# Optimization experiments

Hardware: AMD Instinct MI355X
Metric: run time of the kernel (lower is better)

## Reference

```python
import jax, jax.numpy as jnp
import numpy as np

N = 100000   # nodes
E = 800000   # edges
IN = 128     # in_channels == embedding_size (required by residual Linear)
EMB = 128
OUT = 64
EPS = 1e-5   # GraphNorm eps (PyG default)


def setup_inputs() -> dict:
    key = jax.random.key(0)
    ks = jax.random.split(key, 8)
    x = jax.random.normal(ks[0], (N, IN), jnp.float32)
    edge_index = jax.random.randint(ks[1], (2, E), 0, N, dtype=jnp.int64)
    g = lambda k, shape, scale: jax.random.normal(k, shape, jnp.float32) * scale
    return dict(
        x=x,
        edge_index=edge_index,
        W1=g(ks[2], (IN, EMB), IN ** -0.5), b1=jnp.zeros((EMB,), jnp.float32),
        W2=g(ks[3], (EMB, EMB), EMB ** -0.5), b2=jnp.zeros((EMB,), jnp.float32),
        gn1_w=1.0 + g(ks[4], (EMB,), 0.05), gn1_b=jnp.zeros((EMB,), jnp.float32), gn1_ms=jnp.ones((EMB,), jnp.float32),
        gn2_w=1.0 + g(ks[5], (EMB,), 0.05), gn2_b=jnp.zeros((EMB,), jnp.float32), gn2_ms=jnp.ones((EMB,), jnp.float32),
        Wr=g(ks[6], (EMB, OUT), EMB ** -0.5), br=jnp.zeros((OUT,), jnp.float32),
    )


def _gcn_conv(x, W, b, src, dst, dinv):
    # PyG GCNConv: h = x @ W; out[i] = sum_{(j->i)} dinv[j]*dinv[i]*h[j]; out += bias
    h = x @ W
    norm = (dinv[src] * dinv[dst])[:, None]        # [E+N, 1]
    msg = h[src] * norm                             # gather + scale (irregular)
    out = jax.ops.segment_sum(msg, dst, num_segments=N)  # scatter-add
    return out + b


def _graph_norm(h, w, b, ms):
    # PyG GraphNorm, single graph: mean/var over node dim
    mean = jnp.mean(h, axis=0)
    c = h - ms * mean
    var = jnp.mean(c * c, axis=0)
    return w * c * jax.lax.rsqrt(var + EPS) + b


def reference(x, edge_index, W1, b1, W2, b2, gn1_w, gn1_b, gn1_ms, gn2_w, gn2_b, gn2_ms, Wr, br):
    loops = jnp.arange(N, dtype=edge_index.dtype)
    src = jnp.concatenate([edge_index[0], loops])   # add self-loops
    dst = jnp.concatenate([edge_index[1], loops])
    deg = jax.ops.segment_sum(jnp.ones_like(src, dtype=x.dtype), dst, num_segments=N)
    dinv = jnp.where(deg > 0, jax.lax.rsqrt(jnp.maximum(deg, 1.0)), 0.0)

    # dropout is identity in eval mode
    x1 = jax.nn.relu(_graph_norm(_gcn_conv(x, W1, b1, src, dst, dinv), gn1_w, gn1_b, gn1_ms))
    x2 = jax.nn.relu(_graph_norm(_gcn_conv(x1, W2, b2, src, dst, dinv), gn2_w, gn2_b, gn2_ms))
    return (x1 + x2) @ Wr + br
```

## Files before the change

### kernel.cpp

```cpp
#include <hip/hip_runtime.h>
#include <hip/hip_bf16.h>

typedef __attribute__((ext_vector_type(8))) short bf16x8;
typedef __attribute__((ext_vector_type(4))) float f32x4;
typedef __attribute__((ext_vector_type(2))) float f32x2;
typedef __attribute__((ext_vector_type(4))) unsigned int u32x4;

#define STATS_BLOCKS 256
#define SLOTS 32

__device__ __forceinline__ int coh_load(const int* p){
  return __hip_atomic_load(p, __ATOMIC_RELAXED, __HIP_MEMORY_SCOPE_AGENT);
}
__device__ __forceinline__ unsigned int coh_loadu(const unsigned int* p){
  return __hip_atomic_load(p, __ATOMIC_RELAXED, __HIP_MEMORY_SCOPE_AGENT);
}

__device__ __forceinline__ float bf2f(unsigned short u){
  union { unsigned int i; float f; } v; v.i = ((unsigned int)u) << 16; return v.f;
}
__device__ __forceinline__ unsigned short f2bf(float f){
  union { float f; unsigned int i; } v; v.f = f;
  return (unsigned short)((v.i + 0x7fffu + ((v.i >> 16) & 1u)) >> 16);
}
__device__ __forceinline__ f32x2 bf2x(unsigned int w){
  union { unsigned int i; float f; } lo, hi;
  lo.i = w << 16; hi.i = w & 0xffff0000u;
  f32x2 r; r.x = lo.f; r.y = hi.f; return r;
}


__global__ __launch_bounds__(256) void k_setup(
    const float* __restrict__ W1, const float* __restrict__ W2, const float* __restrict__ Wr,
    unsigned short* __restrict__ wp1, unsigned short* __restrict__ wp2,
    unsigned short* __restrict__ wpr,
    const int* __restrict__ dst, int* __restrict__ hist, int E, int NBUK){
  int b = blockIdx.x;
  if (b < 160){
    int pb = b;
    const float* W; unsigned short* wp; int ncols;
    if (pb < 64)      { W = W1; wp = wp1; ncols = 128; }
    else if (pb < 128){ W = W2; wp = wp2; ncols = 128; pb -= 64; }
    else              { W = Wr; wp = wpr; ncols = 64;  pb -= 128; }
    int idx = pb*256 + threadIdx.x;
    if (idx >= 128*ncols) return;
    int bb = idx & 7, lane = (idx>>3)&63, kk = (idx>>9)&3, ct = idx>>11;
    int k = kk*32 + ((lane>>4)<<3) + bb;
    int c = ct*16 + (lane&15);
    wp[idx] = f2bf(W[k*ncols + c]);
    return;
  }
  int c = b - 160;
  __shared__ int hcnt[256];
  hcnt[threadIdx.x] = 0;
  __syncthreads();
  int per = (E + 255) >> 8;
  int e0 = c*per, e1 = min(E, e0 + per);
  for (int e = e0 + threadIdx.x; e < e1; e += 256)
    atomicAdd(&hcnt[dst[e] >> 9], 1);
  __syncthreads();
  int t = threadIdx.x;
  if (t < NBUK) hist[t*256 + c] = hcnt[t];
}


__global__ __launch_bounds__(256) void k_scanA(int* __restrict__ hist,
                                               int* __restrict__ btot){
  int b = blockIdx.x, t = threadIdx.x;
  int v = hist[b*256 + t];
  __shared__ int sh[256];
  sh[t] = v; __syncthreads();
  for (int o = 1; o < 256; o <<= 1){
    int x = (t >= o) ? sh[t-o] : 0;
    __syncthreads();
    sh[t] += x;
    __syncthreads();
  }
  hist[b*256 + t] = sh[t] - v;
  if (t == 255) btot[b] = sh[255];
}


__global__ __launch_bounds__(256) void k_scatter(const int* __restrict__ src,
    const int* __restrict__ dst, const int* __restrict__ hist,
    const int* __restrict__ btot, unsigned int* __restrict__ ebuf, int E, int NBUK){
  __shared__ int sh[256];
  __shared__ int cursor[256];
  int c = blockIdx.x, t = threadIdx.x;
  int v = (t < NBUK) ? btot[t] : 0;
  sh[t] = v; __syncthreads();
  for (int o = 1; o < 256; o <<= 1){
    int x = (t >= o) ? sh[t-o] : 0;
    __syncthreads();
    sh[t] += x;
    __syncthreads();
  }
  if (t < NBUK) cursor[t] = hist[t*256 + c] + (sh[t] - v);
  __syncthreads();
  int per = (E + 255) >> 8;
  int e0 = c*per, e1 = min(E, e0 + per);
  for (int e = e0 + t; e < e1; e += 256){
    int d = dst[e], s = src[e];
    int bin = d >> 9;
    int pos = atomicAdd(&cursor[bin], 1);
    ebuf[pos] = ((unsigned int)(d & 511) << 17) | (unsigned int)s;
  }
}


__global__ __launch_bounds__(256) void k_bucket(const unsigned int* __restrict__ ebuf,
    const int* __restrict__ btot, int* __restrict__ cur, int* __restrict__ col,
    int N, int NBUK){
  __shared__ int sh[256];
  __shared__ int cnt[512];
  int b = blockIdx.x, t = threadIdx.x;
  int v = (t < NBUK) ? btot[t] : 0;
  sh[t] = v;
  cnt[t] = 0; cnt[t + 256] = 0;
  __syncthreads();
  for (int o = 1; o < 256; o <<= 1){
    int x = (t >= o) ? sh[t-o] : 0;
    __syncthreads();
    sh[t] += x;
    __syncthreads();
  }
  int e1 = sh[b];
  int e0 = e1 - btot[b];
  int base = b << 9;
  for (int e = e0 + t; e < e1; e += 256){
    unsigned int w = coh_loadu(&ebuf[e]);
    int dl = (int)(w >> 17);
    int s  = (int)(w & 0x1FFFFu);
    int p = atomicAdd(&cnt[dl], 1);
    if (p < SLOTS) col[(size_t)(base + dl)*SLOTS + p] = s;
  }
  __syncthreads();
  int d0 = base + t, d1 = base + t + 256;
  if (d0 < N) cur[d0] = cnt[t];
  if (d1 < N) cur[d1] = cnt[t + 256];
}


__global__ __launch_bounds__(256) void k_gemm1(const float* __restrict__ A,
    const unsigned short* __restrict__ wp, const int* __restrict__ cur,
    unsigned short* __restrict__ h, int nTiles){
  int gw = (int)((blockIdx.x*256 + threadIdx.x) >> 6);
  if (gw >= nTiles) return;
  int lane = threadIdx.x & 63;
  int row0 = gw*16;
  int r  = row0 + (lane & 15);
  int kb = (lane >> 4) * 8;
  bf16x8 a[4];
#pragma unroll
  for (int kk = 0; kk < 4; ++kk){
    const float* p = A + (size_t)r*128 + kk*32 + kb;
    f32x4 v0 = *reinterpret_cast<const f32x4*>(p);
    f32x4 v1 = *reinterpret_cast<const f32x4*>(p + 4);
#pragma unroll
    for (int b = 0; b < 4; ++b){ a[kk][b] = (short)f2bf(v0[b]); a[kk][4+b] = (short)f2bf(v1[b]); }
  }
  int cst = lane & 15;
  int rb  = row0 + ((lane >> 4) << 2);
  float dv[4];
#pragma unroll
  for (int b2 = 0; b2 < 4; ++b2) dv[b2] = rsqrtf(1.0f + (float)cur[rb + b2]);
#pragma unroll
  for (int ct = 0; ct < 8; ++ct){
    f32x4 acc = {0.f,0.f,0.f,0.f};
#pragma unroll
    for (int kk = 0; kk < 4; ++kk){
      bf16x8 b = *reinterpret_cast<const bf16x8*>(wp + ((ct*4 + kk)*64 + lane)*8);
      acc = __builtin_amdgcn_mfma_f32_16x16x32_bf16(a[kk], b, acc, 0, 0, 0);
    }
    int c = ct*16 + cst;
#pragma unroll
    for (int b2 = 0; b2 < 4; ++b2)
      h[(size_t)(rb + b2)*128 + c] = f2bf(dv[b2]*acc[b2]);
  }
}


__global__ __launch_bounds__(256) void k_agg(const unsigned short* __restrict__ h,
    const int* __restrict__ cur, const int* col,
    const float* __restrict__ bias, unsigned short* __restrict__ agg, int N){
  int gw = (int)((blockIdx.x*256 + threadIdx.x) >> 6);
  if (gw*2 >= N) return;
  int lane = threadIdx.x & 63;
  int i = gw*2 + (lane >> 5);
  if (i >= N) i = N - 1;
  int q  = (lane >> 4) & 1;
  int cl = lane & 15;
  int base = lane & 32;
  const u32x4* hp = reinterpret_cast<const u32x4*>(h);
  int craw = cur[i];
  int colv = coh_load(&col[(size_t)i*SLOTS + (lane & 31)]);
  int c = min(craw, SLOTS);
  int idx = ((lane & 31) < c) ? colv : i;
  f32x2 a0 = {0.f,0.f}, a1 = {0.f,0.f}, a2 = {0.f,0.f}, a3 = {0.f,0.f};
  int j = 0;
  for (; j + 4 <= c; j += 4){
    int r0 = __shfl(idx, base + j + q);
    int r1 = __shfl(idx, base + j + 2 + q);
    u32x4 v0 = hp[(size_t)r0*16 + cl];
    u32x4 v1 = hp[(size_t)r1*16 + cl];
    a0 += bf2x(v0.x) + bf2x(v1.x);
    a1 += bf2x(v0.y) + bf2x(v1.y);
    a2 += bf2x(v0.z) + bf2x(v1.z);
    a3 += bf2x(v0.w) + bf2x(v1.w);
  }
  int rem = c - j;
  if (rem > 0){
    int r0 = __shfl(idx, base + j + q);
    int r1 = __shfl(idx, base + j + 2 + q);
    if (q < rem){
      u32x4 v0 = hp[(size_t)r0*16 + cl];
      a0 += bf2x(v0.x); a1 += bf2x(v0.y); a2 += bf2x(v0.z); a3 += bf2x(v0.w);
    }
    if (q + 2 < rem){
      u32x4 v1 = hp[(size_t)r1*16 + cl];
      a0 += bf2x(v1.x); a1 += bf2x(v1.y); a2 += bf2x(v1.z); a3 += bf2x(v1.w);
    }
  }
  float acc[8] = {a0.x, a0.y, a1.x, a1.y, a2.x, a2.y, a3.x, a3.y};
#pragma unroll
  for (int b = 0; b < 8; ++b)
    acc[b] += __shfl_xor(acc[b], 16);
  if ((lane & 16) == 0){
    u32x4 hv = hp[(size_t)i*16 + cl];
    float di = rsqrtf(1.0f + (float)craw);
    f32x4 bb0 = *reinterpret_cast<const f32x4*>(bias + cl*8);
    f32x4 bb1 = *reinterpret_cast<const f32x4*>(bias + cl*8 + 4);
    f32x2 s0 = bf2x(hv.x), s1 = bf2x(hv.y), s2 = bf2x(hv.z), s3 = bf2x(hv.w);
    float sf[8] = {s0.x, s0.y, s1.x, s1.y, s2.x, s2.y, s3.x, s3.y};
    float fin[8];
#pragma unroll
    for (int b = 0; b < 4; ++b) fin[b] = di*(acc[b] + sf[b]) + bb0[b];
#pragma unroll
    for (int b = 0; b < 4; ++b) fin[4+b] = di*(acc[4+b] + sf[4+b]) + bb1[b];
    u32x4 ov;
    asm("v_cvt_pk_bf16_f32 %0, %1, %2" : "=v"(ov.x) : "v"(fin[0]), "v"(fin[1]));
    asm("v_cvt_pk_bf16_f32 %0, %1, %2" : "=v"(ov.y) : "v"(fin[2]), "v"(fin[3]));
    asm("v_cvt_pk_bf16_f32 %0, %1, %2" : "=v"(ov.z) : "v"(fin[4]), "v"(fin[5]));
    asm("v_cvt_pk_bf16_f32 %0, %1, %2" : "=v"(ov.w) : "v"(fin[6]), "v"(fin[7]));
    reinterpret_cast<u32x4*>(agg)[(size_t)i*16 + cl] = ov;
  }
}


__global__ __launch_bounds__(256) void k_stats(const unsigned short* __restrict__ agg,
    float* __restrict__ partials, int N){
  int tid = blockIdx.x*256 + threadIdx.x;
  int g = threadIdx.x & 15;
  int c0 = g * 8;
  float S1[8] = {0,0,0,0,0,0,0,0}, S2[8] = {0,0,0,0,0,0,0,0};
  size_t total = (size_t)N * 16;
  for (size_t p = tid; p < total; p += (size_t)STATS_BLOCKS*256){
    bf16x8 v = reinterpret_cast<const bf16x8*>(agg)[p];
#pragma unroll
    for (int b = 0; b < 8; ++b){
      float f = bf2f((unsigned short)v[b]);
      S1[b] += f; S2[b] += f*f;
    }
  }
  __shared__ float sh1[16][128];
  __shared__ float sh2[16][128];
  int cp = threadIdx.x >> 4;
#pragma unroll
  for (int b = 0; b < 8; ++b){ sh1[cp][c0 + b] = S1[b]; sh2[cp][c0 + b] = S2[b]; }
  __syncthreads();
  int t = threadIdx.x;
  if (t < 128){
    float s = 0.f;
#pragma unroll
    for (int qq = 0; qq < 16; ++qq) s += sh1[qq][t];
    partials[blockIdx.x*256 + t] = s;
  } else {
    int cc = t - 128;
    float s = 0.f;
#pragma unroll
    for (int qq = 0; qq < 16; ++qq) s += sh2[qq][cc];
    partials[blockIdx.x*256 + 128 + cc] = s;
  }
}


__global__ void k_reduce(const float* __restrict__ partials, const float* __restrict__ gw_,
    const float* __restrict__ gb_, const float* __restrict__ gms_,
    float* __restrict__ st, int N){
  int t = threadIdx.x;
  float S = 0.f;
#pragma unroll 8
  for (int b = 0; b < STATS_BLOCKS; ++b)
    S += partials[b*256 + t];
  __shared__ float sh[256];
  sh[t] = S;
  __syncthreads();
  if (t >= 128) return;
  int c = t;
  float S1 = sh[c], S2 = sh[128 + c];
  float m  = S1 / (float)N;
  float ms = gms_[c];
  float var = S2/(float)N - 2.f*ms*m*m + ms*ms*m*m;
  float rs = rsqrtf(var + 1e-5f);
  float wv = gw_[c];
  st[c]       = wv * rs;
  st[128 + c] = gb_[c] - wv*rs*ms*m;
}


__global__ __launch_bounds__(256) void k_gemm2(const unsigned short* __restrict__ agg,
    const float* __restrict__ st, const unsigned short* __restrict__ wp,
    const int* __restrict__ cur, unsigned short* __restrict__ h, int nTiles){
  int gw = (int)((blockIdx.x*256 + threadIdx.x) >> 6);
  if (gw >= nTiles) return;
  int lane = threadIdx.x & 63;
  int row0 = gw*16;
  int r  = row0 + (lane & 15);
  int kb = (lane >> 4) * 8;
  bf16x8 a[4];
#pragma unroll
  for (int kk = 0; kk < 4; ++kk){
    int cb = kk*32 + kb;
    bf16x8 v = *reinterpret_cast<const bf16x8*>(agg + (size_t)r*128 + cb);
    f32x4 s0 = *reinterpret_cast<const f32x4*>(st + cb);
    f32x4 s1 = *reinterpret_cast<const f32x4*>(st + cb + 4);
    f32x4 t0 = *reinterpret_cast<const f32x4*>(st + 128 + cb);
    f32x4 t1 = *reinterpret_cast<const f32x4*>(st + 128 + cb + 4);
#pragma unroll
    for (int b = 0; b < 4; ++b){
      a[kk][b]   = (short)f2bf(fmaxf(0.f, s0[b]*bf2f((unsigned short)v[b])   + t0[b]));
      a[kk][4+b] = (short)f2bf(fmaxf(0.f, s1[b]*bf2f((unsigned short)v[4+b]) + t1[b]));
    }
  }
  int cst = lane & 15;
  int rb  = row0 + ((lane >> 4) << 2);
  float dv[4];
#pragma unroll
  for (int b2 = 0; b2 < 4; ++b2) dv[b2] = rsqrtf(1.0f + (float)cur[rb + b2]);
#pragma unroll
  for (int ct = 0; ct < 8; ++ct){
    f32x4 acc = {0.f,0.f,0.f,0.f};
#pragma unroll
    for (int kk = 0; kk < 4; ++kk){
      bf16x8 b = *reinterpret_cast<const bf16x8*>(wp + ((ct*4 + kk)*64 + lane)*8);
      acc = __builtin_amdgcn_mfma_f32_16x16x32_bf16(a[kk], b, acc, 0, 0, 0);
    }
    int c = ct*16 + cst;
#pragma unroll
    for (int b2 = 0; b2 < 4; ++b2)
      h[(size_t)(rb + b2)*128 + c] = f2bf(dv[b2]*acc[b2]);
  }
}


__global__ __launch_bounds__(256) void k_final(const unsigned short* __restrict__ agg1,
    const unsigned short* __restrict__ agg2, const float* __restrict__ st,
    const unsigned short* __restrict__ wp, const float* __restrict__ br,
    float* __restrict__ out, int nTiles){
  int gw = (int)((blockIdx.x*256 + threadIdx.x) >> 6);
  if (gw >= nTiles) return;
  int lane = threadIdx.x & 63;
  int row0 = gw*16;
  int r  = row0 + (lane & 15);
  int kb = (lane >> 4) * 8;
  bf16x8 a[4];
#pragma unroll
  for (int kk = 0; kk < 4; ++kk){
    int cb = kk*32 + kb;
    bf16x8 g1 = *reinterpret_cast<const bf16x8*>(agg1 + (size_t)r*128 + cb);
    bf16x8 g2 = *reinterpret_cast<const bf16x8*>(agg2 + (size_t)r*128 + cb);
#pragma unroll
    for (int b = 0; b < 8; ++b){
      int c = cb + b;
      float x1v = bf2f(f2bf(fmaxf(0.f, st[c]*bf2f((unsigned short)g1[b]) + st[128 + c])));
      float r2  = fmaxf(0.f, st[256 + c]*bf2f((unsigned short)g2[b]) + st[384 + c]);
      a[kk][b] = (short)f2bf(x1v + r2);
    }
  }
  int cst = lane & 15;
  int rb  = row0 + ((lane >> 4) << 2);
#pragma unroll
  for (int ct = 0; ct < 4; ++ct){
    f32x4 acc = {0.f,0.f,0.f,0.f};
#pragma unroll
    for (int kk = 0; kk < 4; ++kk){
      bf16x8 b = *reinterpret_cast<const bf16x8*>(wp + ((ct*4 + kk)*64 + lane)*8);
      acc = __builtin_amdgcn_mfma_f32_16x16x32_bf16(a[kk], b, acc, 0, 0, 0);
    }
    int c = ct*16 + cst;
    float bias = br[c];
#pragma unroll
    for (int b2 = 0; b2 < 4; ++b2)
      out[(size_t)(rb + b2)*64 + c] = acc[b2] + bias;
  }
}


extern "C" void kernel_launch(void* const* d_in, const int* in_sizes, int n_in,
                              void* d_out, int out_size, void* d_ws, size_t ws_size,
                              hipStream_t stream){
  const float* x    = (const float*)d_in[0];
  const int*   ei   = (const int*)d_in[1];
  const float* W1   = (const float*)d_in[2];
  const float* b1   = (const float*)d_in[3];
  const float* W2   = (const float*)d_in[4];
  const float* b2   = (const float*)d_in[5];
  const float* g1w  = (const float*)d_in[6];
  const float* g1b  = (const float*)d_in[7];
  const float* g1ms = (const float*)d_in[8];
  const float* g2w  = (const float*)d_in[9];
  const float* g2b  = (const float*)d_in[10];
  const float* g2ms = (const float*)d_in[11];
  const float* Wr   = (const float*)d_in[12];
  const float* br   = (const float*)d_in[13];
  float* out = (float*)d_out;

  int N = in_sizes[0] / 128;
  int E = in_sizes[1] / 2;
  const int* srcp = ei;
  const int* dstp = ei + E;

  char* w = (char*)d_ws;
  auto alloc = [&](size_t bytes){ char* p = w; w += (bytes + 255) & ~(size_t)255; return p; };
  int*   cur           = (int*)  alloc((size_t)N*4);
  int*   col           = (int*)  alloc((size_t)N*SLOTS*4);
  int*   hist          = (int*)  alloc(256*256*4);
  int*   btot          = (int*)  alloc(256*4);
  unsigned int* ebuf   = (unsigned int*)alloc((size_t)E*4);
  float* partials      = (float*)alloc((size_t)STATS_BLOCKS*256*4);
  float* st            = (float*)alloc(4*128*4);
  unsigned short* wp1  = (unsigned short*)alloc(128*128*2);
  unsigned short* wp2  = (unsigned short*)alloc(128*128*2);
  unsigned short* wpr  = (unsigned short*)alloc(128*64*2);
  unsigned short* h    = (unsigned short*)alloc((size_t)N*128*2);
  unsigned short* agg1 = (unsigned short*)alloc((size_t)N*128*2);
  unsigned short* agg2 = (unsigned short*)alloc((size_t)N*128*2);

  int nTiles = N / 16;
  int gemmBlocks = (nTiles + 3) / 4;
  int NBUK = (N + 511) >> 9;
  int aggBlocks = (N + 7) / 8;

  k_setup  <<<160 + 256, 256, 0, stream>>>(W1, W2, Wr, wp1, wp2, wpr, dstp, hist, E, NBUK);
  k_scanA  <<<NBUK, 256, 0, stream>>>(hist, btot);
  k_scatter<<<256, 256, 0, stream>>>(srcp, dstp, hist, btot, ebuf, E, NBUK);
  k_bucket <<<NBUK, 256, 0, stream>>>(ebuf, btot, cur, col, N, NBUK);

  k_gemm1<<<gemmBlocks, 256, 0, stream>>>(x, wp1, cur, h, nTiles);
  k_agg  <<<aggBlocks, 256, 0, stream>>>(h, cur, col, b1, agg1, N);
  k_stats<<<STATS_BLOCKS, 256, 0, stream>>>(agg1, partials, N);
  k_reduce<<<1, 256, 0, stream>>>(partials, g1w, g1b, g1ms, st, N);

  k_gemm2<<<gemmBlocks, 256, 0, stream>>>(agg1, st, wp2, cur, h, nTiles);
  k_agg  <<<aggBlocks, 256, 0, stream>>>(h, cur, col, b2, agg2, N);
  k_stats<<<STATS_BLOCKS, 256, 0, stream>>>(agg2, partials, N);
  k_reduce<<<1, 256, 0, stream>>>(partials, g2w, g2b, g2ms, st + 256, N);

  k_final<<<gemmBlocks, 256, 0, stream>>>(agg1, agg2, st, wpr, br, out, nTiles);
}
```

Baseline: 206.2 us.

## Fuse GraphNorm statistics into aggregation and remap aggregation to four nodes per wave

The aggregation kernel now handles four nodes per wave, with 16 lanes per node, instead of two nodes split across half-waves. This removes the cross-half shuffle reduction and the partial-tail logic. The per-channel sum and sum-of-squares for GraphNorm are computed in-block from the fp32 results and written as per-block partials, which removes the separate stats pass that re-read the aggregated output. A two-stage reduction (64 blocks, then 1) replaces the single-block reduce. The trade-off is less memory-level parallelism per node, a shared-memory reduction plus syncthreads in every agg block, and a large partials buffer. Stats also now come from pre-rounding fp32 values rather than the stored bf16.

```diff
diff --git a/kernel.cpp b/kernel.cpp
--- a/kernel.cpp
+++ b/kernel.cpp
@@ -6,7 +6,6 @@
 typedef __attribute__((ext_vector_type(2))) float f32x2;
 typedef __attribute__((ext_vector_type(4))) unsigned int u32x4;
 
-#define STATS_BLOCKS 256
 #define SLOTS 32
 
 __device__ __forceinline__ int coh_load(const int* p){
@@ -182,25 +181,29 @@
 
 __global__ __launch_bounds__(256) void k_agg(const unsigned short* __restrict__ h,
     const int* __restrict__ cur, const int* col,
-    const float* __restrict__ bias, unsigned short* __restrict__ agg, int N){
-  int gw = (int)((blockIdx.x*256 + threadIdx.x) >> 6);
-  if (gw*2 >= N) return;
+    const float* __restrict__ bias, unsigned short* __restrict__ agg,
+    float* __restrict__ partials, int N){
   int lane = threadIdx.x & 63;
-  int i = gw*2 + (lane >> 5);
-  if (i >= N) i = N - 1;
-  int q  = (lane >> 4) & 1;
+  int wave = threadIdx.x >> 6;
+  int q  = (lane >> 4) & 3;
   int cl = lane & 15;
-  int base = lane & 32;
+  int base = lane & 48;
+  int i = blockIdx.x*16 + wave*4 + q;
+  bool valid = (i < N);
+  int iq = valid ? i : 0;
   const u32x4* hp = reinterpret_cast<const u32x4*>(h);
-  int craw = cur[i];
-  int colv = coh_load(&col[(size_t)i*SLOTS + (lane & 31)]);
+  int craw = cur[iq];
   int c = min(craw, SLOTS);
-  int idx = ((lane & 31) < c) ? colv : i;
-  f32x2 a0 = {0.f,0.f}, a1 = {0.f,0.f}, a2 = {0.f,0.f}, a3 = {0.f,0.f};
+  int colv0 = coh_load(&col[(size_t)iq*SLOTS + cl]);
+  int colv1 = coh_load(&col[(size_t)iq*SLOTS + 16 + cl]);
+  u32x4 hv = hp[(size_t)iq*16 + cl];
+  f32x2 a0 = bf2x(hv.x), a1 = bf2x(hv.y), a2 = bf2x(hv.z), a3 = bf2x(hv.w);
   int j = 0;
-  for (; j + 4 <= c; j += 4){
-    int r0 = __shfl(idx, base + j + q);
-    int r1 = __shfl(idx, base + j + 2 + q);
+  for (; j + 2 <= c; j += 2){
+    int sv0 = (j     < 16) ? colv0 : colv1;
+    int sv1 = (j + 1 < 16) ? colv0 : colv1;
+    int r0 = __shfl(sv0, base + (j & 15));
+    int r1 = __shfl(sv1, base + ((j + 1) & 15));
     u32x4 v0 = hp[(size_t)r0*16 + cl];
     u32x4 v1 = hp[(size_t)r1*16 + cl];
     a0 += bf2x(v0.x) + bf2x(v1.x);
@@ -208,90 +211,71 @@
     a2 += bf2x(v0.z) + bf2x(v1.z);
     a3 += bf2x(v0.w) + bf2x(v1.w);
   }
-  int rem = c - j;
-  if (rem > 0){
-    int r0 = __shfl(idx, base + j + q);
-    int r1 = __shfl(idx, base + j + 2 + q);
-    if (q < rem){
-      u32x4 v0 = hp[(size_t)r0*16 + cl];
-      a0 += bf2x(v0.x); a1 += bf2x(v0.y); a2 += bf2x(v0.z); a3 += bf2x(v0.w);
-    }
-    if (q + 2 < rem){
-      u32x4 v1 = hp[(size_t)r1*16 + cl];
-      a0 += bf2x(v1.x); a1 += bf2x(v1.y); a2 += bf2x(v1.z); a3 += bf2x(v1.w);
-    }
-  }
-  float acc[8] = {a0.x, a0.y, a1.x, a1.y, a2.x, a2.y, a3.x, a3.y};
-#pragma unroll
-  for (int b = 0; b < 8; ++b)
-    acc[b] += __shfl_xor(acc[b], 16);
-  if ((lane & 16) == 0){
-    u32x4 hv = hp[(size_t)i*16 + cl];
-    float di = rsqrtf(1.0f + (float)craw);
-    f32x4 bb0 = *reinterpret_cast<const f32x4*>(bias + cl*8);
-    f32x4 bb1 = *reinterpret_cast<const f32x4*>(bias + cl*8 + 4);
-    f32x2 s0 = bf2x(hv.x), s1 = bf2x(hv.y), s2 = bf2x(hv.z), s3 = bf2x(hv.w);
-    float sf[8] = {s0.x, s0.y, s1.x, s1.y, s2.x, s2.y, s3.x, s3.y};
-    float fin[8];
-#pragma unroll
-    for (int b = 0; b < 4; ++b) fin[b] = di*(acc[b] + sf[b]) + bb0[b];
-#pragma unroll
-    for (int b = 0; b < 4; ++b) fin[4+b] = di*(acc[4+b] + sf[4+b]) + bb1[b];
-    u32x4 ov;
-    asm("v_cvt_pk_bf16_f32 %0, %1, %2" : "=v"(ov.x) : "v"(fin[0]), "v"(fin[1]));
-    asm("v_cvt_pk_bf16_f32 %0, %1, %2" : "=v"(ov.y) : "v"(fin[2]), "v"(fin[3]));
-    asm("v_cvt_pk_bf16_f32 %0, %1, %2" : "=v"(ov.z) : "v"(fin[4]), "v"(fin[5]));
-    asm("v_cvt_pk_bf16_f32 %0, %1, %2" : "=v"(ov.w) : "v"(fin[6]), "v"(fin[7]));
+  if (j < c){
+    int sv0 = (j < 16) ? colv0 : colv1;
+    int r0 = __shfl(sv0, base + (j & 15));
+    u32x4 v0 = hp[(size_t)r0*16 + cl];
+    a0 += bf2x(v0.x); a1 += bf2x(v0.y); a2 += bf2x(v0.z); a3 += bf2x(v0.w);
+  }
+  float di = rsqrtf(1.0f + (float)craw);
+  f32x4 bb0 = *reinterpret_cast<const f32x4*>(bias + cl*8);
+  f32x4 bb1 = *reinterpret_cast<const f32x4*>(bias + cl*8 + 4);
+  float fin[8];
+  fin[0] = di*a0.x + bb0[0]; fin[1] = di*a0.y + bb0[1];
+  fin[2] = di*a1.x + bb0[2]; fin[3] = di*a1.y + bb0[3];
+  fin[4] = di*a2.x + bb1[0]; fin[5] = di*a2.y + bb1[1];
+  fin[6] = di*a3.x + bb1[2]; fin[7] = di*a3.y + bb1[3];
+  u32x4 ov;
+  asm("v_cvt_pk_bf16_f32 %0, %1, %2" : "=v"(ov.x) : "v"(fin[0]), "v"(fin[1]));
+  asm("v_cvt_pk_bf16_f32 %0, %1, %2" : "=v"(ov.y) : "v"(fin[2]), "v"(fin[3]));
+  asm("v_cvt_pk_bf16_f32 %0, %1, %2" : "=v"(ov.z) : "v"(fin[4]), "v"(fin[5]));
+  asm("v_cvt_pk_bf16_f32 %0, %1, %2" : "=v"(ov.w) : "v"(fin[6]), "v"(fin[7]));
+  if (valid)
     reinterpret_cast<u32x4*>(agg)[(size_t)i*16 + cl] = ov;
-  }
-}
-
-
-__global__ __launch_bounds__(256) void k_stats(const unsigned short* __restrict__ agg,
-    float* __restrict__ partials, int N){
-  int tid = blockIdx.x*256 + threadIdx.x;
-  int g = threadIdx.x & 15;
-  int c0 = g * 8;
-  float S1[8] = {0,0,0,0,0,0,0,0}, S2[8] = {0,0,0,0,0,0,0,0};
-  size_t total = (size_t)N * 16;
-  for (size_t p = tid; p < total; p += (size_t)STATS_BLOCKS*256){
-    bf16x8 v = reinterpret_cast<const bf16x8*>(agg)[p];
-#pragma unroll
-    for (int b = 0; b < 8; ++b){
-      float f = bf2f((unsigned short)v[b]);
-      S1[b] += f; S2[b] += f*f;
-    }
-  }
   __shared__ float sh1[16][128];
   __shared__ float sh2[16][128];
   int cp = threadIdx.x >> 4;
 #pragma unroll
-  for (int b = 0; b < 8; ++b){ sh1[cp][c0 + b] = S1[b]; sh2[cp][c0 + b] = S2[b]; }
+  for (int b = 0; b < 8; ++b){
+    float f = valid ? fin[b] : 0.f;
+    sh1[cp][cl*8 + b] = f;
+    sh2[cp][cl*8 + b] = f*f;
+  }
   __syncthreads();
   int t = threadIdx.x;
   if (t < 128){
     float s = 0.f;
 #pragma unroll
     for (int qq = 0; qq < 16; ++qq) s += sh1[qq][t];
-    partials[blockIdx.x*256 + t] = s;
+    partials[(size_t)blockIdx.x*256 + t] = s;
   } else {
     int cc = t - 128;
     float s = 0.f;
 #pragma unroll
     for (int qq = 0; qq < 16; ++qq) s += sh2[qq][cc];
-    partials[blockIdx.x*256 + 128 + cc] = s;
-  }
-}
-
-
-__global__ void k_reduce(const float* __restrict__ partials, const float* __restrict__ gw_,
+    partials[(size_t)blockIdx.x*256 + 128 + cc] = s;
+  }
+}
+
+
+__global__ __launch_bounds__(256) void k_red1(const float* __restrict__ partials,
+    float* __restrict__ red, int nrows){
+  int t = threadIdx.x;
+  float s = 0.f;
+  for (int r = blockIdx.x; r < nrows; r += 64)
+    s += partials[(size_t)r*256 + t];
+  red[blockIdx.x*256 + t] = s;
+}
+
+
+__global__ void k_red2(const float* __restrict__ red, const float* __restrict__ gw_,
     const float* __restrict__ gb_, const float* __restrict__ gms_,
     float* __restrict__ st, int N){
   int t = threadIdx.x;
   float S = 0.f;
 #pragma unroll 8
-  for (int b = 0; b < STATS_BLOCKS; ++b)
-    S += partials[b*256 + t];
+  for (int b = 0; b < 64; ++b)
+    S += red[b*256 + t];
   __shared__ float sh[256];
   sh[t] = S;
   __syncthreads();
@@ -427,7 +411,9 @@
   int*   hist          = (int*)  alloc(256*256*4);
   int*   btot          = (int*)  alloc(256*4);
   unsigned int* ebuf   = (unsigned int*)alloc((size_t)E*4);
-  float* partials      = (float*)alloc((size_t)STATS_BLOCKS*256*4);
+  int aggBlocks = (N + 15)/16;
+  float* partials      = (float*)alloc((size_t)aggBlocks*256*4);
+  float* red           = (float*)alloc(64*256*4);
   float* st            = (float*)alloc(4*128*4);
   unsigned short* wp1  = (unsigned short*)alloc(128*128*2);
   unsigned short* wp2  = (unsigned short*)alloc(128*128*2);
@@ -439,7 +425,6 @@
   int nTiles = N / 16;
   int gemmBlocks = (nTiles + 3) / 4;
   int NBUK = (N + 511) >> 9;
-  int aggBlocks = (N + 7) / 8;
 
   k_setup  <<<160 + 256, 256, 0, stream>>>(W1, W2, Wr, wp1, wp2, wpr, dstp, hist, E, NBUK);
   k_scanA  <<<NBUK, 256, 0, stream>>>(hist, btot);
@@ -447,14 +432,14 @@
   k_bucket <<<NBUK, 256, 0, stream>>>(ebuf, btot, cur, col, N, NBUK);
 
   k_gemm1<<<gemmBlocks, 256, 0, stream>>>(x, wp1, cur, h, nTiles);
-  k_agg  <<<aggBlocks, 256, 0, stream>>>(h, cur, col, b1, agg1, N);
-  k_stats<<<STATS_BLOCKS, 256, 0, stream>>>(agg1, partials, N);
-  k_reduce<<<1, 256, 0, stream>>>(partials, g1w, g1b, g1ms, st, N);
+  k_agg  <<<aggBlocks, 256, 0, stream>>>(h, cur, col, b1, agg1, partials, N);
+  k_red1 <<<64, 256, 0, stream>>>(partials, red, aggBlocks);
+  k_red2 <<<1, 256, 0, stream>>>(red, g1w, g1b, g1ms, st, N);
 
   k_gemm2<<<gemmBlocks, 256, 0, stream>>>(agg1, st, wp2, cur, h, nTiles);
-  k_agg  <<<aggBlocks, 256, 0, stream>>>(h, cur, col, b2, agg2, N);
-  k_stats<<<STATS_BLOCKS, 256, 0, stream>>>(agg2, partials, N);
-  k_reduce<<<1, 256, 0, stream>>>(partials, g2w, g2b, g2ms, st + 256, N);
+  k_agg  <<<aggBlocks, 256, 0, stream>>>(h, cur, col, b2, agg2, partials, N);
+  k_red1 <<<64, 256, 0, stream>>>(partials, red, aggBlocks);
+  k_red2 <<<1, 256, 0, stream>>>(red, g2w, g2b, g2ms, st + 256, N);
 
   k_final<<<gemmBlocks, 256, 0, stream>>>(agg1, agg2, st, wpr, br, out, nTiles);
 }
```

Measured after the change: 229.3 us (median of 6 runs). 1.11x slower.
